# Kernel tuning notes

Measured on AMD Instinct MI355X. Metric: run time of the kernel, lower is better.

Reference implementation:

```python
import jax, jax.numpy as jnp
import numpy as np

EMB, HEADS = 1024, 16
B, T = 4, 1024

def setup_inputs() -> dict:
    key = jax.random.key(0)
    ks = jax.random.split(key, 6)
    sc = 1.0 / np.sqrt(EMB)
    return {
        "x": jax.random.normal(ks[0], (B, T, EMB), jnp.float32),
        "Wq": jax.random.normal(ks[1], (EMB, EMB), jnp.float32) * sc,
        "Wk": jax.random.normal(ks[2], (EMB, EMB), jnp.float32) * sc,
        "Wv": jax.random.normal(ks[3], (EMB, EMB), jnp.float32) * sc,
        "Wo": jax.random.normal(ks[4], (EMB, EMB), jnp.float32) * sc,
        "bo": jnp.zeros((EMB,), jnp.float32),
    }

def reference(x, Wq, Wk, Wv, Wo, bo):
    b, t, e = x.shape
    h = HEADS
    s = e // h
    # nn.Linear(emb, emb, bias=False): y = x @ W.T
    q = (x @ Wq.T).reshape(b, t, h, s).transpose(0, 2, 1, 3)  # (b,h,t,s)
    k = (x @ Wk.T).reshape(b, t, h, s).transpose(0, 2, 1, 3)
    v = (x @ Wv.T).reshape(b, t, h, s).transpose(0, 2, 1, 3)
    scale = e ** 0.25  # original scales q and k each by emb**(1/4)
    q = q / scale
    k = k / scale
    dot = jnp.einsum('bhqs,bhks->bhqk', q, k)  # (b,h,t,t)
    # causal mask: strict upper triangle -> -inf (mask_diagonal=False)
    causal = jnp.tril(jnp.ones((t, t), dtype=bool))
    dot = jnp.where(causal[None, None], dot, -jnp.inf)
    attn = jax.nn.softmax(dot, axis=-1)
    out = jnp.einsum('bhqk,bhks->bhqs', attn, v)  # (b,h,t,s)
    out = out.transpose(0, 2, 1, 3).reshape(b, t, e)
    return out @ Wo.T + bo
```

## Files before the change

kernel.cpp:

```cpp
#include <hip/hip_runtime.h>
#include <hip/hip_bf16.h>
#include <stdint.h>


typedef __attribute__((ext_vector_type(8))) short short8;
typedef __attribute__((ext_vector_type(4))) float f32x4;
typedef __attribute__((ext_vector_type(16))) float f32x16;

__device__ __forceinline__ unsigned short f2bf(float f) {
    union { float f; unsigned int u; } v; v.f = f;
    unsigned int r = v.u + 0x7FFFu + ((v.u >> 16) & 1u);
    return (unsigned short)(r >> 16);
}

__device__ __forceinline__ void gload_lds16(const ushort* g, ushort* l) {
    __builtin_amdgcn_global_load_lds(
        (const __attribute__((address_space(1))) void*)g,
        (__attribute__((address_space(3))) void*)l,
        16, 0, 0);
}

__device__ __forceinline__ void wait_vmcnt_0() { asm volatile("s_waitcnt vmcnt(0)" ::: "memory"); }
__device__ __forceinline__ void wait_vmcnt_3() { asm volatile("s_waitcnt vmcnt(3)" ::: "memory"); }
__device__ __forceinline__ void wait_vmcnt_4() { asm volatile("s_waitcnt vmcnt(4)" ::: "memory"); }

__device__ __forceinline__ void block_barrier() {
    __builtin_amdgcn_sched_barrier(0);
    __builtin_amdgcn_s_barrier();
    __builtin_amdgcn_sched_barrier(0);
}
__device__ __forceinline__ void lgk0() {
    asm volatile("s_waitcnt lgkmcnt(0)" ::: "memory");
    __builtin_amdgcn_sched_barrier(0);
}

__device__ __forceinline__ unsigned int cvtpk(float lo, float hi) {
    unsigned int r;
    asm("v_cvt_pk_bf16_f32 %0, %1, %2" : "=v"(r) : "v"(lo), "v"(hi));
    return r;
}
__device__ __forceinline__ void plswap(unsigned int& x, unsigned int& y) {
    asm volatile("v_permlane32_swap_b32 %0, %1" : "+v"(x), "+v"(y));
}

__global__ __launch_bounds__(256) void cast_bf16(
    const float* __restrict__ x,  const float* __restrict__ wq,
    const float* __restrict__ wk, const float* __restrict__ wv,
    const float* __restrict__ wo, ushort* __restrict__ dst)
{
    size_t e0 = (size_t)(blockIdx.x * 256 + threadIdx.x) * 4;
    const float* src; size_t off;
    if      (e0 < 4194304u) { src = x;  off = e0; }
    else if (e0 < 5242880u) { src = wq; off = e0 - 4194304u; }
    else if (e0 < 6291456u) { src = wk; off = e0 - 5242880u; }
    else if (e0 < 7340032u) { src = wv; off = e0 - 6291456u; }
    else                    { src = wo; off = e0 - 7340032u; }
    float4 v = *(const float4*)(src + off);
    ushort4 o;
    o.x = f2bf(v.x); o.y = f2bf(v.y); o.z = f2bf(v.z); o.w = f2bf(v.w);
    *(ushort4*)(dst + e0) = o;
}

__global__ __launch_bounds__(512) void gemm_qkv_8ph(
    const ushort* __restrict__ A, const ushort* __restrict__ B,
    ushort* __restrict__ Qf, ushort* __restrict__ Kf, ushort* __restrict__ Vf)
{
    __shared__ ushort lds[2][2][2][128 * 64];

    const int id = blockIdx.x;
    const int swz = (id & 7) * 24 + (id >> 3);
    const int bx = swz % 12, by = swz / 12;
    const int n0 = bx * 256, m0 = by * 256;
    const int t = threadIdx.x, w = t >> 6, l = t & 63;
    const int l15 = l & 15, l4 = l >> 4;
    const int wr = w >> 2, wc = w & 3;
    const int K = 1024;

    auto stage_half = [&](const ushort* gsrc, ushort* dst) {
        #pragma unroll
        for (int i = 0; i < 2; ++i) {
            int slot = i * 512 + t;
            int r = slot >> 3, blk = slot & 7;
            gload_lds16(gsrc + (size_t)r * K + ((blk ^ (r & 7)) << 3),
                        dst + (i * 512 + w * 64) * 8);
        }
    };
    auto stageA = [&](int kt, int h, int buf) {
        stage_half(A + (size_t)(m0 + h * 128) * K + kt * 64, &lds[buf][0][h][0]);
    };
    auto stageB = [&](int kt, int h, int buf) {
        stage_half(B + (size_t)(n0 + h * 128) * K + kt * 64, &lds[buf][1][h][0]);
    };

    short8 af[8];
    short8 vb0[4], vb1[4];
    f32x4 acc[8][4] = {};

    auto readA = [&](int buf, int qm) {
        const ushort* base = &lds[buf][0][wr][0];
        #pragma unroll
        for (int kk = 0; kk < 2; ++kk)
            #pragma unroll
            for (int mt = 0; mt < 4; ++mt) {
                int row = qm * 64 + mt * 16 + l15;
                af[kk * 4 + mt] = *(const short8*)
                    &base[row * 64 + (((kk * 4 + l4) ^ (row & 7)) << 3)];
            }
    };
    auto readB0 = [&](int buf, int qn) {
        const ushort* base = &lds[buf][1][wc >> 1][0];
        #pragma unroll
        for (int kk = 0; kk < 2; ++kk)
            #pragma unroll
            for (int nt = 0; nt < 2; ++nt) {
                int row = (wc & 1) * 64 + qn * 32 + nt * 16 + l15;
                vb0[kk * 2 + nt] = *(const short8*)
                    &base[row * 64 + (((kk * 4 + l4) ^ (row & 7)) << 3)];
            }
    };
    auto readB1 = [&](int buf, int qn) {
        const ushort* base = &lds[buf][1][wc >> 1][0];
        #pragma unroll
        for (int kk = 0; kk < 2; ++kk)
            #pragma unroll
            for (int nt = 0; nt < 2; ++nt) {
                int row = (wc & 1) * 64 + qn * 32 + nt * 16 + l15;
                vb1[kk * 2 + nt] = *(const short8*)
                    &base[row * 64 + (((kk * 4 + l4) ^ (row & 7)) << 3)];
            }
    };
    auto mfma_vb0 = [&](int qm, int qn) {
        __builtin_amdgcn_s_setprio(1);
        #pragma unroll
        for (int kk = 0; kk < 2; ++kk)
            #pragma unroll
            for (int mt = 0; mt < 4; ++mt)
                #pragma unroll
                for (int nt = 0; nt < 2; ++nt)
                    acc[qm * 4 + mt][qn * 2 + nt] =
                        __builtin_amdgcn_mfma_f32_16x16x32_bf16(
                            af[kk * 4 + mt], vb0[kk * 2 + nt],
                            acc[qm * 4 + mt][qn * 2 + nt], 0, 0, 0);
        __builtin_amdgcn_s_setprio(0);
    };
    auto mfma_vb1 = [&](int qm, int qn) {
        __builtin_amdgcn_s_setprio(1);
        #pragma unroll
        for (int kk = 0; kk < 2; ++kk)
            #pragma unroll
            for (int mt = 0; mt < 4; ++mt)
                #pragma unroll
                for (int nt = 0; nt < 2; ++nt)
                    acc[qm * 4 + mt][qn * 2 + nt] =
                        __builtin_amdgcn_mfma_f32_16x16x32_bf16(
                            af[kk * 4 + mt], vb1[kk * 2 + nt],
                            acc[qm * 4 + mt][qn * 2 + nt], 0, 0, 0);
        __builtin_amdgcn_s_setprio(0);
    };

    stageB(0, 0, 0); stageB(0, 1, 0); stageA(0, 0, 0); stageA(0, 1, 0);
    stageB(1, 0, 1); stageB(1, 1, 1);
    wait_vmcnt_4();
    block_barrier();

    for (int j = 0; j < 8; ++j) {
        const bool more = (j < 7);
        readA(0, 0); readB0(0, 0);
        stageA(2 * j + 1, 0, 1);
        block_barrier(); lgk0();
        mfma_vb0(0, 0);
        block_barrier();
        readB1(0, 1);
        stageA(2 * j + 1, 1, 1);
        block_barrier(); lgk0();
        mfma_vb1(0, 1);
        block_barrier();
        readA(0, 1);
        if (more) stageB(2 * j + 2, 0, 0);
        block_barrier(); lgk0();
        mfma_vb1(1, 1);
        block_barrier();
        if (more) stageB(2 * j + 2, 1, 0);
        block_barrier(); lgk0();
        mfma_vb0(1, 0);
        if (more) wait_vmcnt_4(); else wait_vmcnt_0();
        block_barrier();
        readA(1, 0); readB0(1, 0);
        if (more) stageA(2 * j + 2, 0, 0);
        block_barrier(); lgk0();
        mfma_vb0(0, 0);
        block_barrier();
        readB1(1, 1);
        if (more) stageA(2 * j + 2, 1, 0);
        block_barrier(); lgk0();
        mfma_vb1(0, 1);
        block_barrier();
        readA(1, 1);
        if (more) stageB(2 * j + 3, 0, 1);
        block_barrier(); lgk0();
        mfma_vb1(1, 1);
        block_barrier();
        if (more) stageB(2 * j + 3, 1, 1);
        block_barrier(); lgk0();
        mfma_vb0(1, 0);
        if (more) { wait_vmcnt_4(); block_barrier(); }
    }

    #pragma unroll
    for (int qm = 0; qm < 2; ++qm) {
        #pragma unroll
        for (int mt = 0; mt < 4; ++mt) {
            int row = m0 + wr * 128 + qm * 64 + mt * 16 + l4 * 4;
            int b = row >> 10, tok = row & 1023;
            #pragma unroll
            for (int qn = 0; qn < 2; ++qn) {
                #pragma unroll
                for (int nt = 0; nt < 2; ++nt) {
                    int col = n0 + wc * 64 + qn * 32 + nt * 16 + l15;
                    int sel = col >> 10;
                    int cw  = col & 1023;
                    int h = cw >> 6, s = cw & 63;
                    size_t bhb = (size_t)(b * 16 + h) * 65536;
                    f32x4 v = acc[qm * 4 + mt][qn * 2 + nt];
                    if (sel == 2) {
                        size_t off = bhb + (tok >> 6) * 4096 + (s >> 5) * 2048
                                   + ((tok >> 4) & 3) * 512 + ((tok >> 3) & 1) * 256
                                   + (s & 31) * 8 + (tok & 7);
                        ushort4 o;
                        o.x = f2bf(v[0]); o.y = f2bf(v[1]);
                        o.z = f2bf(v[2]); o.w = f2bf(v[3]);
                        *(ushort4*)&Vf[off] = o;
                    } else {
                        ushort* dst = (sel == 0) ? Qf : Kf;
                        float scl = (sel == 0) ? 0.03125f : 1.0f;
                        size_t off = bhb + (tok >> 5) * 2048 + (s >> 4) * 512
                                   + ((s >> 3) & 1) * 256 + (tok & 31) * 8 + (s & 7);
                        #pragma unroll
                        for (int jj = 0; jj < 4; ++jj)
                            dst[off + jj * 8] = f2bf(v[jj] * scl);
                    }
                }
            }
        }
    }
}

template<int MODE, int BM, int WRg, int WCg>
__global__ __launch_bounds__(256) void gemm_bt(
    const ushort* __restrict__ A, const ushort* __restrict__ B,
    float* __restrict__ Cout, const float* __restrict__ bias)
{
    constexpr int MF = BM / (32 * WRg);
    constexpr int NF = 128 / (32 * WCg);
    constexpr int NSTEP = 32;
    const int K = 1024;
    const int n0 = blockIdx.x * 128;
    const int m0 = blockIdx.y * BM;
    const int t  = threadIdx.x;
    const int w  = t >> 6, l = t & 63;
    const int l31 = l & 31, lh = l >> 5;
    const int wr = w / WCg, wc = w % WCg;

    __shared__ ushort As[3 * BM * 32];
    __shared__ ushort Bs[3 * 128 * 32];

    auto stage = [&](int j) {
        const int buf = j % 3;
        const int k0 = j * 32;
        #pragma unroll
        for (int i = 0; i < BM / 64; ++i) {
            int slot = i * 256 + t;
            int r = slot >> 2, blk = slot & 3;
            gload_lds16(A + (size_t)(m0 + r) * K + k0 + ((blk ^ ((r >> 1) & 3)) << 3),
                        &As[buf * BM * 32 + (i * 256 + w * 64) * 8]);
        }
        #pragma unroll
        for (int i = 0; i < 2; ++i) {
            int slot = i * 256 + t;
            int r = slot >> 2, blk = slot & 3;
            gload_lds16(B + (size_t)(n0 + r) * K + k0 + ((blk ^ ((r >> 1) & 3)) << 3),
                        &Bs[buf * 128 * 32 + (i * 256 + w * 64) * 8]);
        }
    };

    f32x16 acc[MF][NF] = {};

    stage(0); stage(1);
    for (int kt = 0; kt < NSTEP; ++kt) {
        if (kt < NSTEP - 1) { if (BM == 128) wait_vmcnt_4(); else wait_vmcnt_3(); }
        else wait_vmcnt_0();
        block_barrier();
        if (kt + 2 < NSTEP) stage(kt + 2);

        const ushort* Ab = &As[(kt % 3) * BM * 32];
        const ushort* Bb = &Bs[(kt % 3) * 128 * 32];
        #pragma unroll
        for (int kk = 0; kk < 2; ++kk) {
            const int c = kk * 2 + lh;
            short8 af[MF], bf[NF];
            #pragma unroll
            for (int mt = 0; mt < MF; ++mt) {
                int row = wr * (MF * 32) + mt * 32 + l31;
                af[mt] = *(const short8*)&Ab[row * 32 + ((c ^ ((row >> 1) & 3)) << 3)];
            }
            #pragma unroll
            for (int nt = 0; nt < NF; ++nt) {
                int row = wc * (NF * 32) + nt * 32 + l31;
                bf[nt] = *(const short8*)&Bb[row * 32 + ((c ^ ((row >> 1) & 3)) << 3)];
            }
            #pragma unroll
            for (int mt = 0; mt < MF; ++mt)
                #pragma unroll
                for (int nt = 0; nt < NF; ++nt)
                    acc[mt][nt] = __builtin_amdgcn_mfma_f32_32x32x16_bf16(
                        af[mt], bf[nt], acc[mt][nt], 0, 0, 0);
        }
    }

    #pragma unroll
    for (int mt = 0; mt < MF; ++mt) {
        int rbase = m0 + wr * (MF * 32) + mt * 32 + 4 * lh;
        #pragma unroll
        for (int nt = 0; nt < NF; ++nt) {
            int col = n0 + wc * (NF * 32) + nt * 32 + l31;
            float bi = bias[col];
            #pragma unroll
            for (int reg = 0; reg < 16; ++reg) {
                int row = rbase + (reg & 3) + 8 * (reg >> 2);
                Cout[(size_t)row * 1024 + col] = acc[mt][nt][reg] + bi;
            }
        }
    }
}

#define PVSTEP(SF, B, VK0, VK1)                                               \
    {                                                                         \
        unsigned int A0_ = cvtpk(SF[(B) + 0], SF[(B) + 1]);                   \
        unsigned int A1_ = cvtpk(SF[(B) + 2], SF[(B) + 3]);                   \
        unsigned int B0_ = cvtpk(SF[(B) + 4], SF[(B) + 5]);                   \
        unsigned int B1_ = cvtpk(SF[(B) + 6], SF[(B) + 7]);                   \
        plswap(A0_, B0_);                                                     \
        plswap(A1_, B1_);                                                     \
        union { unsigned int u[4]; short8 s; } pa_;                           \
        pa_.u[0] = A0_; pa_.u[1] = A1_; pa_.u[2] = B0_; pa_.u[3] = B1_;       \
        accO0 = __builtin_amdgcn_mfma_f32_32x32x16_bf16(pa_.s, VK0, accO0, 0, 0, 0); \
        accO1 = __builtin_amdgcn_mfma_f32_32x32x16_bf16(pa_.s, VK1, accO1, 0, 0, 0); \
    }

#define EXP4(SF, R)                                                           \
    SF[(R) + 0] = __expf(SF[(R) + 0]); ls0 += SF[(R) + 0];                    \
    SF[(R) + 1] = __expf(SF[(R) + 1]); ls1 += SF[(R) + 1];                    \
    SF[(R) + 2] = __expf(SF[(R) + 2]); ls2 += SF[(R) + 2];                    \
    SF[(R) + 3] = __expf(SF[(R) + 3]); ls3 += SF[(R) + 3];

#define MEXP1(SF, R, OFF, LS)                                                 \
    {                                                                         \
        int kv_ = (OFF) + ((R) & 3) + 8 * ((R) >> 2) + 4 * hi;                \
        float e_ = (kv_ > qrow) ? 0.f : __expf(SF[R]);                        \
        SF[R] = e_; LS += e_;                                                 \
    }

#define MEXP16(SF, OFF)                                                       \
    MEXP1(SF, 0, OFF, ls0)  MEXP1(SF, 1, OFF, ls1)                            \
    MEXP1(SF, 2, OFF, ls2)  MEXP1(SF, 3, OFF, ls3)                            \
    MEXP1(SF, 4, OFF, ls0)  MEXP1(SF, 5, OFF, ls1)                            \
    MEXP1(SF, 6, OFF, ls2)  MEXP1(SF, 7, OFF, ls3)                            \
    MEXP1(SF, 8, OFF, ls0)  MEXP1(SF, 9, OFF, ls1)                            \
    MEXP1(SF, 10, OFF, ls2) MEXP1(SF, 11, OFF, ls3)                           \
    MEXP1(SF, 12, OFF, ls0) MEXP1(SF, 13, OFF, ls1)                           \
    MEXP1(SF, 14, OFF, ls2) MEXP1(SF, 15, OFF, ls3)

__global__ __launch_bounds__(64, 2) void attn_kernel(
    const ushort* __restrict__ Qf, const ushort* __restrict__ Kf,
    const ushort* __restrict__ Vf, ushort* __restrict__ O)
{
    const int id = blockIdx.x;
    const int bh = id & 63;
    const int g  = 31 - (id >> 6);
    const int l = threadIdx.x;
    const int l31 = l & 31, hi = l >> 5;

    const ushort* qp = Qf + (size_t)bh * 65536 + (size_t)g * 2048 + (size_t)l * 8;
    const ushort* kp = Kf + (size_t)bh * 65536 + (size_t)l * 8;
    const ushort* vp = Vf + (size_t)bh * 65536 + (size_t)l * 8;

    short8 qb0 = *(const short8*)(qp);
    short8 qb1 = *(const short8*)(qp + 512);
    short8 qb2 = *(const short8*)(qp + 1024);
    short8 qb3 = *(const short8*)(qp + 1536);

    f32x16 accO0 = {}, accO1 = {};
    float ls0 = 0.f, ls1 = 0.f, ls2 = 0.f, ls3 = 0.f;
    const int qrow = g * 32 + l31;
    const int nkv = (g >> 1) + 1;

    for (int kvt = 0; kvt < nkv - 1; ++kvt) {
        const ushort* kt = kp + (size_t)kvt * 4096;
        const ushort* vt = vp + (size_t)kvt * 4096;
        short8 k00 = *(const short8*)(kt);
        short8 k01 = *(const short8*)(kt + 512);
        short8 k02 = *(const short8*)(kt + 1024);
        short8 k03 = *(const short8*)(kt + 1536);
        short8 k10 = *(const short8*)(kt + 2048);
        short8 k11 = *(const short8*)(kt + 2560);
        short8 k12 = *(const short8*)(kt + 3072);
        short8 k13 = *(const short8*)(kt + 3584);
        short8 v00 = *(const short8*)(vt);
        short8 v01 = *(const short8*)(vt + 512);
        short8 v02 = *(const short8*)(vt + 1024);
        short8 v03 = *(const short8*)(vt + 1536);
        short8 v10 = *(const short8*)(vt + 2048);
        short8 v11 = *(const short8*)(vt + 2560);
        short8 v12 = *(const short8*)(vt + 3072);
        short8 v13 = *(const short8*)(vt + 3584);
        __builtin_amdgcn_sched_barrier(0);

        f32x16 sf0 = {}, sf1 = {};
        sf0 = __builtin_amdgcn_mfma_f32_32x32x16_bf16(k00, qb0, sf0, 0, 0, 0);
        sf0 = __builtin_amdgcn_mfma_f32_32x32x16_bf16(k01, qb1, sf0, 0, 0, 0);
        sf0 = __builtin_amdgcn_mfma_f32_32x32x16_bf16(k02, qb2, sf0, 0, 0, 0);
        sf0 = __builtin_amdgcn_mfma_f32_32x32x16_bf16(k03, qb3, sf0, 0, 0, 0);
        sf1 = __builtin_amdgcn_mfma_f32_32x32x16_bf16(k10, qb0, sf1, 0, 0, 0);
        sf1 = __builtin_amdgcn_mfma_f32_32x32x16_bf16(k11, qb1, sf1, 0, 0, 0);
        sf1 = __builtin_amdgcn_mfma_f32_32x32x16_bf16(k12, qb2, sf1, 0, 0, 0);
        sf1 = __builtin_amdgcn_mfma_f32_32x32x16_bf16(k13, qb3, sf1, 0, 0, 0);

        EXP4(sf0, 0) EXP4(sf0, 4) EXP4(sf0, 8) EXP4(sf0, 12)
        EXP4(sf1, 0) EXP4(sf1, 4) EXP4(sf1, 8) EXP4(sf1, 12)

        PVSTEP(sf0, 0, v00, v10)
        PVSTEP(sf0, 8, v01, v11)
        PVSTEP(sf1, 0, v02, v12)
        PVSTEP(sf1, 8, v03, v13)
    }

    {
        const int kvb = (nkv - 1) * 64;
        const ushort* kt = kp + (size_t)(nkv - 1) * 4096;
        const ushort* vt = vp + (size_t)(nkv - 1) * 4096;
        short8 k00 = *(const short8*)(kt);
        short8 k01 = *(const short8*)(kt + 512);
        short8 k02 = *(const short8*)(kt + 1024);
        short8 k03 = *(const short8*)(kt + 1536);
        short8 v00 = *(const short8*)(vt);
        short8 v01 = *(const short8*)(vt + 512);
        short8 v02 = *(const short8*)(vt + 1024);
        short8 v03 = *(const short8*)(vt + 1536);
        short8 v10 = *(const short8*)(vt + 2048);
        short8 v11 = *(const short8*)(vt + 2560);
        short8 v12 = *(const short8*)(vt + 3072);
        short8 v13 = *(const short8*)(vt + 3584);
        __builtin_amdgcn_sched_barrier(0);

        f32x16 sf0 = {};
        sf0 = __builtin_amdgcn_mfma_f32_32x32x16_bf16(k00, qb0, sf0, 0, 0, 0);
        sf0 = __builtin_amdgcn_mfma_f32_32x32x16_bf16(k01, qb1, sf0, 0, 0, 0);
        sf0 = __builtin_amdgcn_mfma_f32_32x32x16_bf16(k02, qb2, sf0, 0, 0, 0);
        sf0 = __builtin_amdgcn_mfma_f32_32x32x16_bf16(k03, qb3, sf0, 0, 0, 0);
        MEXP16(sf0, kvb)
        PVSTEP(sf0, 0, v00, v10)
        PVSTEP(sf0, 8, v01, v11)

        if (g & 1) {
            short8 k10 = *(const short8*)(kt + 2048);
            short8 k11 = *(const short8*)(kt + 2560);
            short8 k12 = *(const short8*)(kt + 3072);
            short8 k13 = *(const short8*)(kt + 3584);
            f32x16 sf1 = {};
            sf1 = __builtin_amdgcn_mfma_f32_32x32x16_bf16(k10, qb0, sf1, 0, 0, 0);
            sf1 = __builtin_amdgcn_mfma_f32_32x32x16_bf16(k11, qb1, sf1, 0, 0, 0);
            sf1 = __builtin_amdgcn_mfma_f32_32x32x16_bf16(k12, qb2, sf1, 0, 0, 0);
            sf1 = __builtin_amdgcn_mfma_f32_32x32x16_bf16(k13, qb3, sf1, 0, 0, 0);
            MEXP16(sf1, kvb + 32)
            PVSTEP(sf1, 0, v02, v12)
            PVSTEP(sf1, 8, v03, v13)
        }
    }

    float lsum = (ls0 + ls1) + (ls2 + ls3);
    float ltot = lsum + __shfl_xor(lsum, 32);
    float inv = 1.0f / ltot;
    const int b = bh >> 4, h = bh & 15;
    #pragma unroll
    for (int r = 0; r < 16; ++r) {
        int qr = (r & 3) + 8 * (r >> 2) + 4 * hi;
        float invr = __shfl(inv, qr);
        int tq = g * 32 + qr;
        O[((size_t)b * 1024 + tq) * 1024 + h * 64 + l31]      = f2bf(accO0[r] * invr);
        O[((size_t)b * 1024 + tq) * 1024 + h * 64 + 32 + l31] = f2bf(accO1[r] * invr);
    }
}

extern "C" void kernel_launch(void* const* d_in, const int* in_sizes, int n_in,
                              void* d_out, int out_size, void* d_ws, size_t ws_size,
                              hipStream_t stream) {
    const float* x  = (const float*)d_in[0];
    const float* wq = (const float*)d_in[1];
    const float* wk = (const float*)d_in[2];
    const float* wv = (const float*)d_in[3];
    const float* wo = (const float*)d_in[4];
    const float* bo = (const float*)d_in[5];
    float* out = (float*)d_out;

    ushort* ws  = (ushort*)d_ws;
    ushort* xb  = ws;
    ushort* wb  = ws + (4u << 20);
    ushort* Qfb = ws + (8u << 20);
    ushort* Kfb = ws + (12u << 20);
    ushort* Vfb = ws + (16u << 20);
    ushort* Ob  = ws + (20u << 20);

    cast_bf16<<<8192, 256, 0, stream>>>(x, wq, wk, wv, wo, ws);
    gemm_qkv_8ph<<<192, 512, 0, stream>>>(xb, wb, Qfb, Kfb, Vfb);
    attn_kernel<<<2048, 64, 0, stream>>>(Qfb, Kfb, Vfb, Ob);
    gemm_bt<1, 64, 1, 4><<<dim3(8, 64), 256, 0, stream>>>(
        Ob, wb + (3u << 20), out, bo);
}
```

Before: 84.98 us.

## Double-buffer K/V register loads to prefetch next tile during compute

The attention kernel now holds two register sets of K/V fragments and issues the global loads for the next KV tile before computing on the current one. The loop is unrolled by two with ping-pong buffers, and the diagonal tile is handled by a masked compute macro. This is meant to hide global-load latency behind the MFMA and exp work of the previous tile. It doubles the registers used for K/V, which could raise register pressure or cause spills under the launch bound of two waves. The diagonal tile now always loads the upper K half even when it is unused.

```diff
diff --git a/kernel.cpp b/kernel.cpp
--- a/kernel.cpp
+++ b/kernel.cpp
@@ -370,6 +370,65 @@
     MEXP1(SF, 12, OFF, ls0) MEXP1(SF, 13, OFF, ls1)                           \
     MEXP1(SF, 14, OFF, ls2) MEXP1(SF, 15, OFF, ls3)
 
+#define LOADSET(P, KT, VT)                                                    \
+    k##P##0 = *(const short8*)(KT);                                           \
+    k##P##1 = *(const short8*)((KT) + 512);                                   \
+    k##P##2 = *(const short8*)((KT) + 1024);                                  \
+    k##P##3 = *(const short8*)((KT) + 1536);                                  \
+    k##P##4 = *(const short8*)((KT) + 2048);                                  \
+    k##P##5 = *(const short8*)((KT) + 2560);                                  \
+    k##P##6 = *(const short8*)((KT) + 3072);                                  \
+    k##P##7 = *(const short8*)((KT) + 3584);                                  \
+    v##P##0 = *(const short8*)(VT);                                           \
+    v##P##1 = *(const short8*)((VT) + 512);                                   \
+    v##P##2 = *(const short8*)((VT) + 1024);                                  \
+    v##P##3 = *(const short8*)((VT) + 1536);                                  \
+    v##P##4 = *(const short8*)((VT) + 2048);                                  \
+    v##P##5 = *(const short8*)((VT) + 2560);                                  \
+    v##P##6 = *(const short8*)((VT) + 3072);                                  \
+    v##P##7 = *(const short8*)((VT) + 3584);
+
+#define COMPUTE_FREE(P)                                                       \
+    {                                                                         \
+        f32x16 sf0 = {}, sf1 = {};                                            \
+        sf0 = __builtin_amdgcn_mfma_f32_32x32x16_bf16(k##P##0, qb0, sf0, 0, 0, 0); \
+        sf0 = __builtin_amdgcn_mfma_f32_32x32x16_bf16(k##P##1, qb1, sf0, 0, 0, 0); \
+        sf0 = __builtin_amdgcn_mfma_f32_32x32x16_bf16(k##P##2, qb2, sf0, 0, 0, 0); \
+        sf0 = __builtin_amdgcn_mfma_f32_32x32x16_bf16(k##P##3, qb3, sf0, 0, 0, 0); \
+        sf1 = __builtin_amdgcn_mfma_f32_32x32x16_bf16(k##P##4, qb0, sf1, 0, 0, 0); \
+        sf1 = __builtin_amdgcn_mfma_f32_32x32x16_bf16(k##P##5, qb1, sf1, 0, 0, 0); \
+        sf1 = __builtin_amdgcn_mfma_f32_32x32x16_bf16(k##P##6, qb2, sf1, 0, 0, 0); \
+        sf1 = __builtin_amdgcn_mfma_f32_32x32x16_bf16(k##P##7, qb3, sf1, 0, 0, 0); \
+        EXP4(sf0, 0) EXP4(sf0, 4) EXP4(sf0, 8) EXP4(sf0, 12)                  \
+        EXP4(sf1, 0) EXP4(sf1, 4) EXP4(sf1, 8) EXP4(sf1, 12)                  \
+        PVSTEP(sf0, 0, v##P##0, v##P##4)                                      \
+        PVSTEP(sf0, 8, v##P##1, v##P##5)                                      \
+        PVSTEP(sf1, 0, v##P##2, v##P##6)                                      \
+        PVSTEP(sf1, 8, v##P##3, v##P##7)                                      \
+    }
+
+#define COMPUTE_DIAG(P, KVB)                                                  \
+    {                                                                         \
+        f32x16 sf0 = {};                                                      \
+        sf0 = __builtin_amdgcn_mfma_f32_32x32x16_bf16(k##P##0, qb0, sf0, 0, 0, 0); \
+        sf0 = __builtin_amdgcn_mfma_f32_32x32x16_bf16(k##P##1, qb1, sf0, 0, 0, 0); \
+        sf0 = __builtin_amdgcn_mfma_f32_32x32x16_bf16(k##P##2, qb2, sf0, 0, 0, 0); \
+        sf0 = __builtin_amdgcn_mfma_f32_32x32x16_bf16(k##P##3, qb3, sf0, 0, 0, 0); \
+        MEXP16(sf0, KVB)                                                      \
+        PVSTEP(sf0, 0, v##P##0, v##P##4)                                      \
+        PVSTEP(sf0, 8, v##P##1, v##P##5)                                      \
+        if (g & 1) {                                                          \
+            f32x16 sf1 = {};                                                  \
+            sf1 = __builtin_amdgcn_mfma_f32_32x32x16_bf16(k##P##4, qb0, sf1, 0, 0, 0); \
+            sf1 = __builtin_amdgcn_mfma_f32_32x32x16_bf16(k##P##5, qb1, sf1, 0, 0, 0); \
+            sf1 = __builtin_amdgcn_mfma_f32_32x32x16_bf16(k##P##6, qb2, sf1, 0, 0, 0); \
+            sf1 = __builtin_amdgcn_mfma_f32_32x32x16_bf16(k##P##7, qb3, sf1, 0, 0, 0); \
+            MEXP16(sf1, (KVB) + 32)                                           \
+            PVSTEP(sf1, 0, v##P##2, v##P##6)                                  \
+            PVSTEP(sf1, 8, v##P##3, v##P##7)                                  \
+        }                                                                     \
+    }
+
 __global__ __launch_bounds__(64, 2) void attn_kernel(
     const ushort* __restrict__ Qf, const ushort* __restrict__ Kf,
     const ushort* __restrict__ Vf, ushort* __restrict__ O)
@@ -394,87 +453,33 @@
     const int qrow = g * 32 + l31;
     const int nkv = (g >> 1) + 1;
 
-    for (int kvt = 0; kvt < nkv - 1; ++kvt) {
-        const ushort* kt = kp + (size_t)kvt * 4096;
-        const ushort* vt = vp + (size_t)kvt * 4096;
-        short8 k00 = *(const short8*)(kt);
-        short8 k01 = *(const short8*)(kt + 512);
-        short8 k02 = *(const short8*)(kt + 1024);
-        short8 k03 = *(const short8*)(kt + 1536);
-        short8 k10 = *(const short8*)(kt + 2048);
-        short8 k11 = *(const short8*)(kt + 2560);
-        short8 k12 = *(const short8*)(kt + 3072);
-        short8 k13 = *(const short8*)(kt + 3584);
-        short8 v00 = *(const short8*)(vt);
-        short8 v01 = *(const short8*)(vt + 512);
-        short8 v02 = *(const short8*)(vt + 1024);
-        short8 v03 = *(const short8*)(vt + 1536);
-        short8 v10 = *(const short8*)(vt + 2048);
-        short8 v11 = *(const short8*)(vt + 2560);
-        short8 v12 = *(const short8*)(vt + 3072);
-        short8 v13 = *(const short8*)(vt + 3584);
+    short8 kA0, kA1, kA2, kA3, kA4, kA5, kA6, kA7;
+    short8 vA0, vA1, vA2, vA3, vA4, vA5, vA6, vA7;
+    short8 kB0, kB1, kB2, kB3, kB4, kB5, kB6, kB7;
+    short8 vB0, vB1, vB2, vB3, vB4, vB5, vB6, vB7;
+
+    LOADSET(A, kp, vp)
+    __builtin_amdgcn_sched_barrier(0);
+
+    int kvt = 0;
+    while (kvt + 1 < nkv) {
+        LOADSET(B, kp + (size_t)(kvt + 1) * 4096, vp + (size_t)(kvt + 1) * 4096)
         __builtin_amdgcn_sched_barrier(0);
-
-        f32x16 sf0 = {}, sf1 = {};
-        sf0 = __builtin_amdgcn_mfma_f32_32x32x16_bf16(k00, qb0, sf0, 0, 0, 0);
-        sf0 = __builtin_amdgcn_mfma_f32_32x32x16_bf16(k01, qb1, sf0, 0, 0, 0);
-        sf0 = __builtin_amdgcn_mfma_f32_32x32x16_bf16(k02, qb2, sf0, 0, 0, 0);
-        sf0 = __builtin_amdgcn_mfma_f32_32x32x16_bf16(k03, qb3, sf0, 0, 0, 0);
-        sf1 = __builtin_amdgcn_mfma_f32_32x32x16_bf16(k10, qb0, sf1, 0, 0, 0);
-        sf1 = __builtin_amdgcn_mfma_f32_32x32x16_bf16(k11, qb1, sf1, 0, 0, 0);
-        sf1 = __builtin_amdgcn_mfma_f32_32x32x16_bf16(k12, qb2, sf1, 0, 0, 0);
-        sf1 = __builtin_amdgcn_mfma_f32_32x32x16_bf16(k13, qb3, sf1, 0, 0, 0);
-
-        EXP4(sf0, 0) EXP4(sf0, 4) EXP4(sf0, 8) EXP4(sf0, 12)
-        EXP4(sf1, 0) EXP4(sf1, 4) EXP4(sf1, 8) EXP4(sf1, 12)
-
-        PVSTEP(sf0, 0, v00, v10)
-        PVSTEP(sf0, 8, v01, v11)
-        PVSTEP(sf1, 0, v02, v12)
-        PVSTEP(sf1, 8, v03, v13)
-    }
-
-    {
-        const int kvb = (nkv - 1) * 64;
-        const ushort* kt = kp + (size_t)(nkv - 1) * 4096;
-        const ushort* vt = vp + (size_t)(nkv - 1) * 4096;
-        short8 k00 = *(const short8*)(kt);
-        short8 k01 = *(const short8*)(kt + 512);
-        short8 k02 = *(const short8*)(kt + 1024);
-        short8 k03 = *(const short8*)(kt + 1536);
-        short8 v00 = *(const short8*)(vt);
-        short8 v01 = *(const short8*)(vt + 512);
-        short8 v02 = *(const short8*)(vt + 1024);
-        short8 v03 = *(const short8*)(vt + 1536);
-        short8 v10 = *(const short8*)(vt + 2048);
-        short8 v11 = *(const short8*)(vt + 2560);
-        short8 v12 = *(const short8*)(vt + 3072);
-        short8 v13 = *(const short8*)(vt + 3584);
-        __builtin_amdgcn_sched_barrier(0);
-
-        f32x16 sf0 = {};
-        sf0 = __builtin_amdgcn_mfma_f32_32x32x16_bf16(k00, qb0, sf0, 0, 0, 0);
-        sf0 = __builtin_amdgcn_mfma_f32_32x32x16_bf16(k01, qb1, sf0, 0, 0, 0);
-        sf0 = __builtin_amdgcn_mfma_f32_32x32x16_bf16(k02, qb2, sf0, 0, 0, 0);
-        sf0 = __builtin_amdgcn_mfma_f32_32x32x16_bf16(k03, qb3, sf0, 0, 0, 0);
-        MEXP16(sf0, kvb)
-        PVSTEP(sf0, 0, v00, v10)
-        PVSTEP(sf0, 8, v01, v11)
-
-        if (g & 1) {
-            short8 k10 = *(const short8*)(kt + 2048);
-            short8 k11 = *(const short8*)(kt + 2560);
-            short8 k12 = *(const short8*)(kt + 3072);
-            short8 k13 = *(const short8*)(kt + 3584);
-            f32x16 sf1 = {};
-            sf1 = __builtin_amdgcn_mfma_f32_32x32x16_bf16(k10, qb0, sf1, 0, 0, 0);
-            sf1 = __builtin_amdgcn_mfma_f32_32x32x16_bf16(k11, qb1, sf1, 0, 0, 0);
-            sf1 = __builtin_amdgcn_mfma_f32_32x32x16_bf16(k12, qb2, sf1, 0, 0, 0);
-            sf1 = __builtin_amdgcn_mfma_f32_32x32x16_bf16(k13, qb3, sf1, 0, 0, 0);
-            MEXP16(sf1, kvb + 32)
-            PVSTEP(sf1, 0, v02, v12)
-            PVSTEP(sf1, 8, v03, v13)
-        }
+        COMPUTE_FREE(A)
+        ++kvt;
+        if (kvt + 1 < nkv) {
+            LOADSET(A, kp + (size_t)(kvt + 1) * 4096, vp + (size_t)(kvt + 1) * 4096)
+            __builtin_amdgcn_sched_barrier(0);
+            COMPUTE_FREE(B)
+            ++kvt;
+        } else {
+            COMPUTE_DIAG(B, kvt * 64)
+            ++kvt;
+            break;
+        }
+    }
+    if (kvt < nkv) {
+        COMPUTE_DIAG(A, kvt * 64)
     }
 
     float lsum = (ls0 + ls1) + (ls2 + ls3);
```

After: 125.4 us. 47.6% more time.

## Share K/V tiles across two query waves via double-buffered LDS staging

Applied to the files above, without the earlier changes.

The attention kernel now runs two 64-lane waves per block, one for each adjacent 32-row query group that shares the same KV range. K/V tiles are loaded into a double-buffered LDS ring with direct global-to-LDS loads, prefetching two tiles ahead. Each wave then reads its fragments from LDS instead of re-fetching them from global memory. Block order is also serpentine-permuted so work is balanced across the causal triangle. This halves global K/V traffic per query group and overlaps loads with compute, at the cost of block barriers, LDS use, and fewer total blocks.

```diff
diff --git a/kernel.cpp b/kernel.cpp
--- a/kernel.cpp
+++ b/kernel.cpp
@@ -23,6 +23,7 @@
 __device__ __forceinline__ void wait_vmcnt_0() { asm volatile("s_waitcnt vmcnt(0)" ::: "memory"); }
 __device__ __forceinline__ void wait_vmcnt_3() { asm volatile("s_waitcnt vmcnt(3)" ::: "memory"); }
 __device__ __forceinline__ void wait_vmcnt_4() { asm volatile("s_waitcnt vmcnt(4)" ::: "memory"); }
+__device__ __forceinline__ void wait_vmcnt_8() { asm volatile("s_waitcnt vmcnt(8)" ::: "memory"); }
 
 __device__ __forceinline__ void block_barrier() {
     __builtin_amdgcn_sched_barrier(0);
@@ -370,111 +371,117 @@
     MEXP1(SF, 12, OFF, ls0) MEXP1(SF, 13, OFF, ls1)                           \
     MEXP1(SF, 14, OFF, ls2) MEXP1(SF, 15, OFF, ls3)
 
-__global__ __launch_bounds__(64, 2) void attn_kernel(
+__global__ __launch_bounds__(128, 2) void attn_kernel(
     const ushort* __restrict__ Qf, const ushort* __restrict__ Kf,
     const ushort* __restrict__ Vf, ushort* __restrict__ O)
 {
+    __shared__ ushort kvlds[2][8192];
+
     const int id = blockIdx.x;
     const int bh = id & 63;
-    const int g  = 31 - (id >> 6);
-    const int l = threadIdx.x;
+    const int j = id >> 6;
+    const int m = j >> 2, a = j & 3;
+    const int u = 4 * m + ((m & 1) ? 3 - a : a);
+    const int t128 = threadIdx.x;
+    const int w = t128 >> 6, l = t128 & 63;
+    const int g = 2 * u + w;
     const int l31 = l & 31, hi = l >> 5;
+    const int nkv = u + 1;
+    const int qrow = g * 32 + l31;
 
     const ushort* qp = Qf + (size_t)bh * 65536 + (size_t)g * 2048 + (size_t)l * 8;
-    const ushort* kp = Kf + (size_t)bh * 65536 + (size_t)l * 8;
-    const ushort* vp = Vf + (size_t)bh * 65536 + (size_t)l * 8;
+    const ushort* kg = Kf + (size_t)bh * 65536;
+    const ushort* vg = Vf + (size_t)bh * 65536;
 
     short8 qb0 = *(const short8*)(qp);
     short8 qb1 = *(const short8*)(qp + 512);
     short8 qb2 = *(const short8*)(qp + 1024);
     short8 qb3 = *(const short8*)(qp + 1536);
 
+    auto stage = [&](int buf, int t) {
+        const ushort* ks = kg + (size_t)t * 4096;
+        const ushort* vs = vg + (size_t)t * 4096;
+        #pragma unroll
+        for (int i = 0; i < 4; ++i)
+            gload_lds16(ks + (size_t)(i * 128 + t128) * 8,
+                        &kvlds[buf][(i * 128 + w * 64) * 8]);
+        #pragma unroll
+        for (int i = 0; i < 4; ++i)
+            gload_lds16(vs + (size_t)(i * 128 + t128) * 8,
+                        &kvlds[buf][4096 + (i * 128 + w * 64) * 8]);
+    };
+
     f32x16 accO0 = {}, accO1 = {};
     float ls0 = 0.f, ls1 = 0.f, ls2 = 0.f, ls3 = 0.f;
-    const int qrow = g * 32 + l31;
-    const int nkv = (g >> 1) + 1;
-
-    for (int kvt = 0; kvt < nkv - 1; ++kvt) {
-        const ushort* kt = kp + (size_t)kvt * 4096;
-        const ushort* vt = vp + (size_t)kvt * 4096;
-        short8 k00 = *(const short8*)(kt);
-        short8 k01 = *(const short8*)(kt + 512);
-        short8 k02 = *(const short8*)(kt + 1024);
-        short8 k03 = *(const short8*)(kt + 1536);
-        short8 k10 = *(const short8*)(kt + 2048);
-        short8 k11 = *(const short8*)(kt + 2560);
-        short8 k12 = *(const short8*)(kt + 3072);
-        short8 k13 = *(const short8*)(kt + 3584);
-        short8 v00 = *(const short8*)(vt);
-        short8 v01 = *(const short8*)(vt + 512);
-        short8 v02 = *(const short8*)(vt + 1024);
-        short8 v03 = *(const short8*)(vt + 1536);
-        short8 v10 = *(const short8*)(vt + 2048);
-        short8 v11 = *(const short8*)(vt + 2560);
-        short8 v12 = *(const short8*)(vt + 3072);
-        short8 v13 = *(const short8*)(vt + 3584);
-        __builtin_amdgcn_sched_barrier(0);
-
-        f32x16 sf0 = {}, sf1 = {};
-        sf0 = __builtin_amdgcn_mfma_f32_32x32x16_bf16(k00, qb0, sf0, 0, 0, 0);
-        sf0 = __builtin_amdgcn_mfma_f32_32x32x16_bf16(k01, qb1, sf0, 0, 0, 0);
-        sf0 = __builtin_amdgcn_mfma_f32_32x32x16_bf16(k02, qb2, sf0, 0, 0, 0);
-        sf0 = __builtin_amdgcn_mfma_f32_32x32x16_bf16(k03, qb3, sf0, 0, 0, 0);
-        sf1 = __builtin_amdgcn_mfma_f32_32x32x16_bf16(k10, qb0, sf1, 0, 0, 0);
-        sf1 = __builtin_amdgcn_mfma_f32_32x32x16_bf16(k11, qb1, sf1, 0, 0, 0);
-        sf1 = __builtin_amdgcn_mfma_f32_32x32x16_bf16(k12, qb2, sf1, 0, 0, 0);
-        sf1 = __builtin_amdgcn_mfma_f32_32x32x16_bf16(k13, qb3, sf1, 0, 0, 0);
-
-        EXP4(sf0, 0) EXP4(sf0, 4) EXP4(sf0, 8) EXP4(sf0, 12)
-        EXP4(sf1, 0) EXP4(sf1, 4) EXP4(sf1, 8) EXP4(sf1, 12)
-
-        PVSTEP(sf0, 0, v00, v10)
-        PVSTEP(sf0, 8, v01, v11)
-        PVSTEP(sf1, 0, v02, v12)
-        PVSTEP(sf1, 8, v03, v13)
-    }
-
-    {
-        const int kvb = (nkv - 1) * 64;
-        const ushort* kt = kp + (size_t)(nkv - 1) * 4096;
-        const ushort* vt = vp + (size_t)(nkv - 1) * 4096;
-        short8 k00 = *(const short8*)(kt);
-        short8 k01 = *(const short8*)(kt + 512);
-        short8 k02 = *(const short8*)(kt + 1024);
-        short8 k03 = *(const short8*)(kt + 1536);
-        short8 v00 = *(const short8*)(vt);
-        short8 v01 = *(const short8*)(vt + 512);
-        short8 v02 = *(const short8*)(vt + 1024);
-        short8 v03 = *(const short8*)(vt + 1536);
-        short8 v10 = *(const short8*)(vt + 2048);
-        short8 v11 = *(const short8*)(vt + 2560);
-        short8 v12 = *(const short8*)(vt + 3072);
-        short8 v13 = *(const short8*)(vt + 3584);
-        __builtin_amdgcn_sched_barrier(0);
-
-        f32x16 sf0 = {};
-        sf0 = __builtin_amdgcn_mfma_f32_32x32x16_bf16(k00, qb0, sf0, 0, 0, 0);
-        sf0 = __builtin_amdgcn_mfma_f32_32x32x16_bf16(k01, qb1, sf0, 0, 0, 0);
-        sf0 = __builtin_amdgcn_mfma_f32_32x32x16_bf16(k02, qb2, sf0, 0, 0, 0);
-        sf0 = __builtin_amdgcn_mfma_f32_32x32x16_bf16(k03, qb3, sf0, 0, 0, 0);
-        MEXP16(sf0, kvb)
-        PVSTEP(sf0, 0, v00, v10)
-        PVSTEP(sf0, 8, v01, v11)
-
-        if (g & 1) {
-            short8 k10 = *(const short8*)(kt + 2048);
-            short8 k11 = *(const short8*)(kt + 2560);
-            short8 k12 = *(const short8*)(kt + 3072);
-            short8 k13 = *(const short8*)(kt + 3584);
-            f32x16 sf1 = {};
+
+    stage(0, 0);
+    if (nkv > 1) { stage(1, 1); wait_vmcnt_8(); } else { wait_vmcnt_0(); }
+    block_barrier();
+
+    for (int t = 0; t < nkv; ++t) {
+        const ushort* kb = &kvlds[t & 1][0];
+        const ushort* vb = &kvlds[t & 1][4096];
+        short8 k00 = *(const short8*)(kb + l * 8);
+        short8 k01 = *(const short8*)(kb + 512 + l * 8);
+        short8 k02 = *(const short8*)(kb + 1024 + l * 8);
+        short8 k03 = *(const short8*)(kb + 1536 + l * 8);
+        short8 k10 = *(const short8*)(kb + 2048 + l * 8);
+        short8 k11 = *(const short8*)(kb + 2560 + l * 8);
+        short8 k12 = *(const short8*)(kb + 3072 + l * 8);
+        short8 k13 = *(const short8*)(kb + 3584 + l * 8);
+        short8 v00 = *(const short8*)(vb + l * 8);
+        short8 v01 = *(const short8*)(vb + 512 + l * 8);
+        short8 v02 = *(const short8*)(vb + 1024 + l * 8);
+        short8 v03 = *(const short8*)(vb + 1536 + l * 8);
+        short8 v10 = *(const short8*)(vb + 2048 + l * 8);
+        short8 v11 = *(const short8*)(vb + 2560 + l * 8);
+        short8 v12 = *(const short8*)(vb + 3072 + l * 8);
+        short8 v13 = *(const short8*)(vb + 3584 + l * 8);
+        lgk0();
+        block_barrier();
+        if (t + 2 < nkv) stage(t & 1, t + 2);
+
+        if (t < nkv - 1) {
+            f32x16 sf0 = {}, sf1 = {};
+            sf0 = __builtin_amdgcn_mfma_f32_32x32x16_bf16(k00, qb0, sf0, 0, 0, 0);
+            sf0 = __builtin_amdgcn_mfma_f32_32x32x16_bf16(k01, qb1, sf0, 0, 0, 0);
+            sf0 = __builtin_amdgcn_mfma_f32_32x32x16_bf16(k02, qb2, sf0, 0, 0, 0);
+            sf0 = __builtin_amdgcn_mfma_f32_32x32x16_bf16(k03, qb3, sf0, 0, 0, 0);
             sf1 = __builtin_amdgcn_mfma_f32_32x32x16_bf16(k10, qb0, sf1, 0, 0, 0);
             sf1 = __builtin_amdgcn_mfma_f32_32x32x16_bf16(k11, qb1, sf1, 0, 0, 0);
             sf1 = __builtin_amdgcn_mfma_f32_32x32x16_bf16(k12, qb2, sf1, 0, 0, 0);
             sf1 = __builtin_amdgcn_mfma_f32_32x32x16_bf16(k13, qb3, sf1, 0, 0, 0);
-            MEXP16(sf1, kvb + 32)
+            EXP4(sf0, 0) EXP4(sf0, 4) EXP4(sf0, 8) EXP4(sf0, 12)
+            EXP4(sf1, 0) EXP4(sf1, 4) EXP4(sf1, 8) EXP4(sf1, 12)
+            PVSTEP(sf0, 0, v00, v10)
+            PVSTEP(sf0, 8, v01, v11)
             PVSTEP(sf1, 0, v02, v12)
             PVSTEP(sf1, 8, v03, v13)
-        }
+        } else {
+            const int kvb = t * 64;
+            f32x16 sf0 = {};
+            sf0 = __builtin_amdgcn_mfma_f32_32x32x16_bf16(k00, qb0, sf0, 0, 0, 0);
+            sf0 = __builtin_amdgcn_mfma_f32_32x32x16_bf16(k01, qb1, sf0, 0, 0, 0);
+            sf0 = __builtin_amdgcn_mfma_f32_32x32x16_bf16(k02, qb2, sf0, 0, 0, 0);
+            sf0 = __builtin_amdgcn_mfma_f32_32x32x16_bf16(k03, qb3, sf0, 0, 0, 0);
+            MEXP16(sf0, kvb)
+            PVSTEP(sf0, 0, v00, v10)
+            PVSTEP(sf0, 8, v01, v11)
+            if (g & 1) {
+                f32x16 sf1 = {};
+                sf1 = __builtin_amdgcn_mfma_f32_32x32x16_bf16(k10, qb0, sf1, 0, 0, 0);
+                sf1 = __builtin_amdgcn_mfma_f32_32x32x16_bf16(k11, qb1, sf1, 0, 0, 0);
+                sf1 = __builtin_amdgcn_mfma_f32_32x32x16_bf16(k12, qb2, sf1, 0, 0, 0);
+                sf1 = __builtin_amdgcn_mfma_f32_32x32x16_bf16(k13, qb3, sf1, 0, 0, 0);
+                MEXP16(sf1, kvb + 32)
+                PVSTEP(sf1, 0, v02, v12)
+                PVSTEP(sf1, 8, v03, v13)
+            }
+        }
+
+        if (t + 2 < nkv) wait_vmcnt_8();
+        else if (t + 1 < nkv) wait_vmcnt_0();
+        block_barrier();
     }
 
     float lsum = (ls0 + ls1) + (ls2 + ls3);
@@ -512,7 +519,7 @@
 
     cast_bf16<<<8192, 256, 0, stream>>>(x, wq, wk, wv, wo, ws);
     gemm_qkv_8ph<<<192, 512, 0, stream>>>(xb, wb, Qfb, Kfb, Vfb);
-    attn_kernel<<<2048, 64, 0, stream>>>(Qfb, Kfb, Vfb, Ob);
+    attn_kernel<<<1024, 128, 0, stream>>>(Qfb, Kfb, Vfb, Ob);
     gemm_bt<1, 64, 1, 4><<<dim3(8, 64), 256, 0, stream>>>(
         Ob, wb + (3u << 20), out, bo);
 }
```

Result: slower. 90.21 us (+6.2%).
